# Optimization experiments

Measured on AMD Instinct MI355X. Metric: run time of the kernel, lower is better.

Reference implementation:

```python
import jax, jax.numpy as jnp
import numpy as np

N_NODES = 50000
N_EDGES = 640000
IN_F, HID, OUT = 128, 128, 64
EPS = 1e-5


def _glorot(key, shape):
    fan_in, fan_out = shape
    lim = jnp.sqrt(6.0 / (fan_in + fan_out))
    return jax.random.uniform(key, shape, jnp.float32, -lim, lim)


def setup_inputs() -> dict:
    key = jax.random.key(0)
    ks = jax.random.split(key, 16)
    inp = {
        "x": jax.random.normal(ks[0], (N_NODES, IN_F), jnp.float32),
        "src": jax.random.randint(ks[1], (N_EDGES,), 0, N_NODES, jnp.int32),
        "dst": jax.random.randint(ks[2], (N_EDGES,), 0, N_NODES, jnp.int32),
        # layer 0: in -> hid
        "Ws0": _glorot(ks[3], (IN_F, HID)),
        "Wn0": _glorot(ks[4], (IN_F, HID)),
        "b0": jnp.zeros((HID,), jnp.float32),
        # layer 1: hid -> hid
        "Ws1": _glorot(ks[5], (HID, HID)),
        "Wn1": _glorot(ks[6], (HID, HID)),
        "b1": jnp.zeros((HID,), jnp.float32),
        # layer 2: hid -> out
        "Ws2": _glorot(ks[7], (HID, OUT)),
        "Wn2": _glorot(ks[8], (HID, OUT)),
        "b2": jnp.zeros((OUT,), jnp.float32),
        # batchnorm params for the two hidden layers
        "g0": jnp.ones((HID,), jnp.float32),
        "beta0": jnp.zeros((HID,), jnp.float32),
        "g1": jnp.ones((HID,), jnp.float32),
        "beta1": jnp.zeros((HID,), jnp.float32),
    }
    return inp


def _sage_conv(h, src, dst, Ws, Wn, b):
    # mean aggregation over in-neighbors (DGL SAGEConv 'mean')
    ones = jnp.ones_like(dst, dtype=h.dtype)
    deg = jax.ops.segment_sum(ones, dst, num_segments=N_NODES)
    agg = jax.ops.segment_sum(h[src], dst, num_segments=N_NODES)
    agg = agg / jnp.maximum(deg, 1.0)[:, None]
    return h @ Ws + agg @ Wn + b


def _batchnorm(h, gamma, beta):
    mu = jnp.mean(h, axis=0)
    var = jnp.mean(jnp.square(h - mu), axis=0)  # biased, like torch BN
    return (h - mu) * jax.lax.rsqrt(var + EPS) * gamma + beta


def reference(x, src, dst, Ws0, Wn0, b0, Ws1, Wn1, b1, Ws2, Wn2, b2,
              g0, beta0, g1, beta1):
    h = _sage_conv(x, src, dst, Ws0, Wn0, b0)
    h = jax.nn.relu(_batchnorm(h, g0, beta0))  # dropout = identity (eval)
    h = _sage_conv(h, src, dst, Ws1, Wn1, b1)
    h = jax.nn.relu(_batchnorm(h, g1, beta1))
    h = _sage_conv(h, src, dst, Ws2, Wn2, b2)
    return h
```

## Files before the change

### kernel.cpp

```cpp
#include <hip/hip_runtime.h>

#define N_NODES 50000
#define N_EDGES 640000
#define EPS 1e-5f
#define NBLK_SCAN 196
#define CGRID 3125

typedef __attribute__((ext_vector_type(8))) short short8;
typedef __attribute__((ext_vector_type(4))) float f32x4;

__device__ inline unsigned short f2bf(float f) {
    unsigned u = __float_as_uint(f);
    u += 0x7fffu + ((u >> 16) & 1u);
    return (unsigned short)(u >> 16);
}
__device__ inline float bf2f(unsigned short b) {
    return __uint_as_float(((unsigned)b) << 16);
}
__device__ inline void storev(short* p, float v) { *(unsigned short*)p = f2bf(v); }
__device__ inline void storev(float* p, float v) { *p = v; }

__global__ void hist_kernel(const int* __restrict__ dst, int* __restrict__ counts,
                            int* __restrict__ erank) {
    int i = blockIdx.x * 256 + threadIdx.x;
    if (i >= N_EDGES / 8) return;
    int4 a = ((const int4*)dst)[2 * i];
    int4 b = ((const int4*)dst)[2 * i + 1];
    int4 ra, rb;
    ra.x = atomicAdd(&counts[a.x], 1);
    ra.y = atomicAdd(&counts[a.y], 1);
    ra.z = atomicAdd(&counts[a.z], 1);
    ra.w = atomicAdd(&counts[a.w], 1);
    rb.x = atomicAdd(&counts[b.x], 1);
    rb.y = atomicAdd(&counts[b.y], 1);
    rb.z = atomicAdd(&counts[b.z], 1);
    rb.w = atomicAdd(&counts[b.w], 1);
    ((int4*)erank)[2 * i]     = ra;
    ((int4*)erank)[2 * i + 1] = rb;
}

__global__ void scan1_kernel(const int* __restrict__ counts, int* __restrict__ incl,
                             int* __restrict__ bsums) {
    __shared__ int tmp[256];
    int t = threadIdx.x;
    int i = blockIdx.x * 256 + t;
    tmp[t] = (i < N_NODES) ? counts[i] : 0;
    __syncthreads();
    for (int off = 1; off < 256; off <<= 1) {
        int add = (t >= off) ? tmp[t - off] : 0;
        __syncthreads();
        tmp[t] += add;
        __syncthreads();
    }
    if (i < N_NODES) incl[i] = tmp[t];
    if (t == 255) bsums[blockIdx.x] = tmp[255];
}

__global__ void scan2_kernel(const int* __restrict__ bsums, int* __restrict__ boff) {
    __shared__ int tmp[256];
    int t = threadIdx.x;
    tmp[t] = (t < NBLK_SCAN) ? bsums[t] : 0;
    __syncthreads();
    for (int off = 1; off < 256; off <<= 1) {
        int add = (t >= off) ? tmp[t - off] : 0;
        __syncthreads();
        tmp[t] += add;
        __syncthreads();
    }
    if (t < NBLK_SCAN) boff[t] = (t == 0) ? 0 : tmp[t - 1];
}

__global__ void scan3_kernel(const int* __restrict__ counts, const int* __restrict__ incl,
                             const int* __restrict__ boff, int* __restrict__ rowptr,
                             float* __restrict__ rdeg) {
    int i = blockIdx.x * 256 + threadIdx.x;
    if (i >= N_NODES) return;
    int c = counts[i];
    int inc = incl[i] + boff[blockIdx.x];
    rowptr[i] = inc - c;
    rdeg[i] = 1.0f / fmaxf((float)c, 1.0f);
    if (i == N_NODES - 1) rowptr[N_NODES] = inc;
}

__global__ void fill_kernel(const int* __restrict__ src, const int* __restrict__ dst,
                            const int* __restrict__ erank, const int* __restrict__ rowptr,
                            int* __restrict__ esrc) {
    int i = blockIdx.x * 256 + threadIdx.x;
    if (i >= N_EDGES / 8) return;
    int4 da = ((const int4*)dst)[2 * i];
    int4 db = ((const int4*)dst)[2 * i + 1];
    int4 sa = ((const int4*)src)[2 * i];
    int4 sb = ((const int4*)src)[2 * i + 1];
    int4 ra = ((const int4*)erank)[2 * i];
    int4 rb = ((const int4*)erank)[2 * i + 1];
    esrc[rowptr[da.x] + ra.x] = sa.x;
    esrc[rowptr[da.y] + ra.y] = sa.y;
    esrc[rowptr[da.z] + ra.z] = sa.z;
    esrc[rowptr[da.w] + ra.w] = sa.w;
    esrc[rowptr[db.x] + rb.x] = sb.x;
    esrc[rowptr[db.y] + rb.y] = sb.y;
    esrc[rowptr[db.z] + rb.z] = sb.z;
    esrc[rowptr[db.w] + rb.w] = sb.w;
}

__global__ void prep_kernel(const float* __restrict__ in, short* __restrict__ outp,
                            int* __restrict__ counts, float* __restrict__ stats,
                            const float* __restrict__ W0, const float* __restrict__ W1,
                            const float* __restrict__ W2, const float* __restrict__ W3,
                            const float* __restrict__ W4, const float* __restrict__ W5,
                            short* __restrict__ P0, short* __restrict__ P1,
                            short* __restrict__ P2, short* __restrict__ P3,
                            short* __restrict__ P4, short* __restrict__ P5) {
    int bi = blockIdx.x, t = threadIdx.x;
    if (bi < CGRID) {
        if (bi == 0 && t < 128) {
            float4 z = make_float4(0.f, 0.f, 0.f, 0.f);
            ((float4*)stats)[t] = z;
        }
        if (bi >= 1 && bi <= NBLK_SCAN) {
            int idx = (bi - 1) * 256 + t;
            if (idx < N_NODES) counts[idx] = 0;
        }
        int i = bi * 256 + t;
        if (i >= N_NODES * 16) return;
        const float4* p = (const float4*)in + 2 * (size_t)i;
        float4 a = p[0], b = p[1];
        short8 v;
        v[0] = (short)f2bf(a.x); v[1] = (short)f2bf(a.y);
        v[2] = (short)f2bf(a.z); v[3] = (short)f2bf(a.w);
        v[4] = (short)f2bf(b.x); v[5] = (short)f2bf(b.y);
        v[6] = (short)f2bf(b.z); v[7] = (short)f2bf(b.w);
        *((short8*)outp + i) = v;
        return;
    }
    int b = bi - CGRID;
    const float* W; short* P; int NC; int base;
    if      (b < 8)  { W = W0; P = P0; NC = 128; base = 0;  }
    else if (b < 16) { W = W1; P = P1; NC = 128; base = 8;  }
    else if (b < 24) { W = W2; P = P2; NC = 128; base = 16; }
    else if (b < 32) { W = W3; P = P3; NC = 128; base = 24; }
    else if (b < 36) { W = W4; P = P4; NC = 64;  base = 32; }
    else             { W = W5; P = P5; NC = 64;  base = 36; }
    int idx = (b - base) * 256 + t;
    int total = 4 * (NC / 16) * 64;
    if (idx >= total) return;
    int lane = idx & 63;
    int cbks = idx >> 6;
    int cb = cbks % (NC / 16);
    int ks = cbks / (NC / 16);
    int col = cb * 16 + (lane & 15);
    int k0 = ks * 32 + ((lane >> 4) << 3);
    short8 v;
    #pragma unroll
    for (int j = 0; j < 8; ++j) v[j] = (short)f2bf(W[(size_t)(k0 + j) * NC + col]);
    *((short8*)P + idx) = v;
}

template<bool BN>
__global__ void gather_k(const short* __restrict__ h, const int* __restrict__ rowptr,
                         const int* __restrict__ esrc, const float* __restrict__ rdeg,
                         const float* __restrict__ sums, const float* __restrict__ sqs,
                         const float* __restrict__ g, const float* __restrict__ beta,
                         short* __restrict__ agg) {
    int node = blockIdx.x * 4 + (threadIdx.x >> 6);
    int lane = threadIdx.x & 63;
    if (node >= N_NODES) return;
    int beg = rowptr[node], end = rowptr[node + 1];
    float s0 = 0.f, s1 = 0.f, b0 = 0.f, b1 = 0.f;
    if (BN) {
        const float invN = 1.0f / N_NODES;
        float2 sm = *(const float2*)(sums + lane * 2);
        float2 sq = *(const float2*)(sqs + lane * 2);
        float2 gg = *(const float2*)(g + lane * 2);
        float2 bb = *(const float2*)(beta + lane * 2);
        float m0 = sm.x * invN, m1 = sm.y * invN;
        float v0 = sq.x * invN - m0 * m0, v1 = sq.y * invN - m1 * m1;
        s0 = rsqrtf(v0 + EPS) * gg.x;
        s1 = rsqrtf(v1 + EPS) * gg.y;
        b0 = bb.x - m0 * s0;
        b1 = bb.y - m1 * s1;
    }
    float ax = 0.f, ay = 0.f;
    while (beg < end) {
        int cnt = min(end - beg, 64);
        int mi = esrc[beg + min(lane, cnt - 1)];
        for (int j = 0; j < cnt; j += 16) {
            int lim = cnt - j; if (lim > 16) lim = 16;
            unsigned v[16];
            #pragma unroll
            for (int u = 0; u < 16; ++u) {
                int s = __shfl(mi, j + (u < lim ? u : lim - 1));
                v[u] = *(const unsigned*)(h + (size_t)s * 128 + lane * 2);
            }
            #pragma unroll
            for (int u = 0; u < 16; ++u) {
                if (u < lim) {
                    float lo = __uint_as_float(v[u] << 16);
                    float hi = __uint_as_float(v[u] & 0xffff0000u);
                    if (BN) {
                        lo = fmaxf(fmaf(lo, s0, b0), 0.f);
                        hi = fmaxf(fmaf(hi, s1, b1), 0.f);
                    }
                    ax += lo; ay += hi;
                }
            }
        }
        beg += cnt;
    }
    float r = rdeg[node];
    unsigned o = ((unsigned)f2bf(ay * r) << 16) | (unsigned)f2bf(ax * r);
    *(unsigned*)(agg + (size_t)node * 128 + lane * 2) = o;
}

template<int NC, bool BNIN, bool STATS, typename OUT>
__global__ __launch_bounds__(512, 4)
void sage_mfma(const short* __restrict__ h, const short* __restrict__ agg,
               const short* __restrict__ Wpk,
               const float* __restrict__ bias,
               const float* __restrict__ sums_in, const float* __restrict__ sqs_in,
               const float* __restrict__ g_in, const float* __restrict__ beta_in,
               float* __restrict__ sums, float* __restrict__ sqs,
               OUT* __restrict__ out) {
    constexpr int CBF = NC / 16;
    constexpr int WSH8 = CBF * 256;
    __shared__ short8 wlds[2 * WSH8];
    __shared__ float ls[128], lq[128];
    const int t = threadIdx.x;
    const int lane = t & 63;
    const int w = t >> 6;
    const int wrow = blockIdx.x * 128 + w * 16;
    const int arow = wrow + (lane & 15);
    const int koff = (lane >> 4) << 3;

    {
        const short8* gw = (const short8*)Wpk;
        #pragma unroll
        for (int i = 0; i < (2 * WSH8) / 512; ++i)
            wlds[t + i * 512] = gw[t + i * 512];
    }
    if (BNIN) {
        if (t < 128) {
            const float invN = 1.0f / N_NODES;
            float m = sums_in[t] * invN;
            float v = sqs_in[t] * invN - m * m;
            float sc = rsqrtf(v + EPS) * g_in[t];
            ls[t] = sc;
            lq[t] = beta_in[t] - m * sc;
        }
    }
    __syncthreads();

    short8 zero8 = {0, 0, 0, 0, 0, 0, 0, 0};
    short8 A[8];
    if (arow < N_NODES) {
        const short8* hb = (const short8*)(h + (size_t)arow * 128 + koff);
        const short8* ab = (const short8*)(agg + (size_t)arow * 128 + koff);
        #pragma unroll
        for (int ks = 0; ks < 4; ++ks) {
            A[ks] = hb[ks * 4];
            A[4 + ks] = ab[ks * 4];
        }
        if (BNIN) {
            #pragma unroll
            for (int ks = 0; ks < 4; ++ks) {
                int base = ks * 32 + koff;
                float4 sc0 = *(const float4*)&ls[base];
                float4 sc1 = *(const float4*)&ls[base + 4];
                float4 sh0 = *(const float4*)&lq[base];
                float4 sh1 = *(const float4*)&lq[base + 4];
                float scv[8] = {sc0.x, sc0.y, sc0.z, sc0.w, sc1.x, sc1.y, sc1.z, sc1.w};
                float shv[8] = {sh0.x, sh0.y, sh0.z, sh0.w, sh1.x, sh1.y, sh1.z, sh1.w};
                short8 v = A[ks];
                #pragma unroll
                for (int j = 0; j < 8; ++j) {
                    float f = bf2f((unsigned short)v[j]);
                    f = fmaxf(fmaf(f, scv[j], shv[j]), 0.f);
                    v[j] = (short)f2bf(f);
                }
                A[ks] = v;
            }
        }
    } else {
        #pragma unroll
        for (int s = 0; s < 8; ++s) A[s] = zero8;
    }

    if (STATS) {
        if (BNIN) __syncthreads();
        if (t < NC) { ls[t] = 0.f; lq[t] = 0.f; }
        __syncthreads();
    }

    f32x4 zacc = {0.f, 0.f, 0.f, 0.f};
    f32x4 acc[CBF];
    #pragma unroll
    for (int c = 0; c < CBF; ++c) acc[c] = zacc;

    #pragma unroll
    for (int s = 0; s < 8; ++s) {
        const int base = (s < 4) ? s * CBF * 64 : WSH8 + (s - 4) * CBF * 64;
        short8 af = A[s];
        #pragma unroll
        for (int c = 0; c < CBF; ++c) {
            short8 b = wlds[base + c * 64 + lane];
            acc[c] = __builtin_amdgcn_mfma_f32_16x16x32_bf16(af, b, acc[c], 0, 0, 0);
        }
    }

    const int col16 = lane & 15;
    const int rbase = wrow + ((lane >> 4) << 2);
    #pragma unroll
    for (int c = 0; c < CBF; ++c) {
        int gcol = c * 16 + col16;
        float bb = bias[gcol];
        float ps = 0.f, pq = 0.f;
        #pragma unroll
        for (int r = 0; r < 4; ++r) {
            int row = rbase + r;
            if (row < N_NODES) {
                float val = acc[c][r] + bb;
                storev(out + (size_t)row * NC + gcol, val);
                if (STATS) { ps += val; pq += val * val; }
            }
        }
        if (STATS) {
            ps += __shfl_xor(ps, 16); ps += __shfl_xor(ps, 32);
            pq += __shfl_xor(pq, 16); pq += __shfl_xor(pq, 32);
            if (lane < 16) {
                atomicAdd(&ls[gcol], ps);
                atomicAdd(&lq[gcol], pq);
            }
        }
    }
    if (STATS) {
        __syncthreads();
        if (t < NC) {
            atomicAdd(&sums[t], ls[t]);
            atomicAdd(&sqs[t], lq[t]);
        }
    }
}

__global__ __launch_bounds__(512, 4)
void sage_mfma2(const short* __restrict__ h, const short* __restrict__ Wpk,
                const float* __restrict__ bias,
                const float* __restrict__ sums_in, const float* __restrict__ sqs_in,
                const float* __restrict__ g_in, const float* __restrict__ beta_in,
                float* __restrict__ out, short* __restrict__ z2) {
    constexpr int CBF = 4;
    constexpr int WSH8 = 1024;
    __shared__ short8 wlds[2 * WSH8];
    __shared__ float ls[128], lq[128];
    const int t = threadIdx.x;
    const int lane = t & 63;
    const int w = t >> 6;
    const int wrow = blockIdx.x * 128 + w * 16;
    const int arow = wrow + (lane & 15);
    const int koff = (lane >> 4) << 3;

    {
        const short8* gw = (const short8*)Wpk;
        #pragma unroll
        for (int i = 0; i < (2 * WSH8) / 512; ++i)
            wlds[t + i * 512] = gw[t + i * 512];
    }
    if (t < 128) {
        const float invN = 1.0f / N_NODES;
        float m = sums_in[t] * invN;
        float v = sqs_in[t] * invN - m * m;
        float sc = rsqrtf(v + EPS) * g_in[t];
        ls[t] = sc;
        lq[t] = beta_in[t] - m * sc;
    }
    __syncthreads();

    short8 zero8 = {0, 0, 0, 0, 0, 0, 0, 0};
    short8 A[4];
    if (arow < N_NODES) {
        const short8* hb = (const short8*)(h + (size_t)arow * 128 + koff);
        #pragma unroll
        for (int ks = 0; ks < 4; ++ks) {
            int base = ks * 32 + koff;
            float4 sc0 = *(const float4*)&ls[base];
            float4 sc1 = *(const float4*)&ls[base + 4];
            float4 sh0 = *(const float4*)&lq[base];
            float4 sh1 = *(const float4*)&lq[base + 4];
            float scv[8] = {sc0.x, sc0.y, sc0.z, sc0.w, sc1.x, sc1.y, sc1.z, sc1.w};
            float shv[8] = {sh0.x, sh0.y, sh0.z, sh0.w, sh1.x, sh1.y, sh1.z, sh1.w};
            short8 v = hb[ks * 4];
            #pragma unroll
            for (int j = 0; j < 8; ++j) {
                float f = bf2f((unsigned short)v[j]);
                f = fmaxf(fmaf(f, scv[j], shv[j]), 0.f);
                v[j] = (short)f2bf(f);
            }
            A[ks] = v;
        }
    } else {
        #pragma unroll
        for (int s = 0; s < 4; ++s) A[s] = zero8;
    }

    f32x4 zacc = {0.f, 0.f, 0.f, 0.f};
    f32x4 accy[CBF], accz[CBF];
    #pragma unroll
    for (int c = 0; c < CBF; ++c) { accy[c] = zacc; accz[c] = zacc; }

    #pragma unroll
    for (int s = 0; s < 4; ++s) {
        short8 af = A[s];
        #pragma unroll
        for (int c = 0; c < CBF; ++c) {
            short8 by = wlds[s * 256 + c * 64 + lane];
            accy[c] = __builtin_amdgcn_mfma_f32_16x16x32_bf16(af, by, accy[c], 0, 0, 0);
        }
        #pragma unroll
        for (int c = 0; c < CBF; ++c) {
            short8 bz = wlds[WSH8 + s * 256 + c * 64 + lane];
            accz[c] = __builtin_amdgcn_mfma_f32_16x16x32_bf16(af, bz, accz[c], 0, 0, 0);
        }
    }

    const int col16 = lane & 15;
    const int rbase = wrow + ((lane >> 4) << 2);
    #pragma unroll
    for (int c = 0; c < CBF; ++c) {
        int gcol = c * 16 + col16;
        float bb = bias[gcol];
        #pragma unroll
        for (int r = 0; r < 4; ++r) {
            int row = rbase + r;
            if (row < N_NODES) {
                out[(size_t)row * 64 + gcol] = accy[c][r] + bb;
                storev(z2 + (size_t)row * 64 + gcol, accz[c][r]);
            }
        }
    }
}

__global__ void gather64_add(const short* __restrict__ z2, const int* __restrict__ rowptr,
                             const int* __restrict__ esrc, const float* __restrict__ rdeg,
                             float* __restrict__ out) {
    int node = blockIdx.x * 4 + (threadIdx.x >> 6);
    int lane = threadIdx.x & 63;
    if (node >= N_NODES) return;
    const int e = lane >> 5;
    const int p = lane & 31;
    int beg = rowptr[node], end = rowptr[node + 1];
    float a0 = 0.f, a1 = 0.f;
    while (beg < end) {
        int cnt = min(end - beg, 64);
        int mi = esrc[beg + min(lane, cnt - 1)];
        for (int j = 0; j < cnt; j += 16) {
            unsigned v[8];
            #pragma unroll
            for (int u = 0; u < 8; ++u) {
                int idx = j + 2 * u + e;
                int s = __shfl(mi, min(idx, cnt - 1));
                v[u] = *(const unsigned*)(z2 + (size_t)s * 64 + p * 2);
            }
            #pragma unroll
            for (int u = 0; u < 8; ++u) {
                int idx = j + 2 * u + e;
                if (idx < cnt) {
                    a0 += __uint_as_float(v[u] << 16);
                    a1 += __uint_as_float(v[u] & 0xffff0000u);
                }
            }
        }
        beg += cnt;
    }
    a0 += __shfl_xor(a0, 32);
    a1 += __shfl_xor(a1, 32);
    if (e == 0) {
        float r = rdeg[node];
        float2* po = (float2*)(out + (size_t)node * 64 + p * 2);
        float2 y = *po;
        y.x += a0 * r;
        y.y += a1 * r;
        *po = y;
    }
}

extern "C" void kernel_launch(void* const* d_in, const int* in_sizes, int n_in,
                              void* d_out, int out_size, void* d_ws, size_t ws_size,
                              hipStream_t stream) {
    const float* x   = (const float*)d_in[0];
    const int*   src = (const int*)d_in[1];
    const int*   dst = (const int*)d_in[2];
    const float* Ws0 = (const float*)d_in[3];
    const float* Wn0 = (const float*)d_in[4];
    const float* b0  = (const float*)d_in[5];
    const float* Ws1 = (const float*)d_in[6];
    const float* Wn1 = (const float*)d_in[7];
    const float* b1  = (const float*)d_in[8];
    const float* Ws2 = (const float*)d_in[9];
    const float* Wn2 = (const float*)d_in[10];
    const float* b2  = (const float*)d_in[11];
    const float* g0  = (const float*)d_in[12];
    const float* bt0 = (const float*)d_in[13];
    const float* g1  = (const float*)d_in[14];
    const float* bt1 = (const float*)d_in[15];

    char* ws = (char*)d_ws;
    const size_t HB2 = (size_t)N_NODES * 128 * 2;
    size_t off = 0;
    short* xb     = (short*)(ws + off); off += HB2;
    short* aggb   = (short*)(ws + off); off += HB2;
    short* h1b    = (short*)(ws + off); off += HB2;
    short* h2b    = (short*)(ws + off); off += HB2;
    short* z2b    = (short*)(ws + off); off += (size_t)N_NODES * 64 * 2;
    int*   esrc   = (int*)(ws + off);   off += (size_t)N_EDGES * 4;
    int*   erank  = (int*)(ws + off);   off += (size_t)N_EDGES * 4;
    int*   counts = (int*)(ws + off);   off += 200192;
    int*   incl   = (int*)(ws + off);   off += 200192;
    int*   rowptr = (int*)(ws + off);   off += 200704;
    float* rdeg   = (float*)(ws + off); off += 200192;
    int*   bsums  = (int*)(ws + off);   off += 1024;
    int*   boff   = (int*)(ws + off);   off += 1024;
    float* stats  = (float*)(ws + off); off += 2048;
    float* sums0  = stats;
    float* sqs0   = stats + 128;
    float* sums1  = stats + 256;
    float* sqs1   = stats + 384;
    short* pW0    = (short*)(ws + off); off += 65536;
    short* pW1    = (short*)(ws + off); off += 65536;
    short* pW2    = (short*)(ws + off); off += 32768;

    float* out = (float*)d_out;

    const int e8grid = (N_EDGES / 8 + 255) / 256;
    const int ggrid  = (N_NODES + 3) / 4;
    const int mgrid  = (N_NODES + 127) / 128;

    prep_kernel<<<CGRID + 40, 256, 0, stream>>>(
        x, xb, counts, stats, Ws0, Wn0, Ws1, Wn1, Ws2, Wn2,
        pW0, pW0 + 16384, pW1, pW1 + 16384, pW2, pW2 + 8192);
    hist_kernel<<<e8grid, 256, 0, stream>>>(dst, counts, erank);
    scan1_kernel<<<NBLK_SCAN, 256, 0, stream>>>(counts, incl, bsums);
    scan2_kernel<<<1, 256, 0, stream>>>(bsums, boff);
    scan3_kernel<<<NBLK_SCAN, 256, 0, stream>>>(counts, incl, boff, rowptr, rdeg);
    fill_kernel<<<e8grid, 256, 0, stream>>>(src, dst, erank, rowptr, esrc);

    gather_k<false><<<ggrid, 256, 0, stream>>>(xb, rowptr, esrc, rdeg,
                                               nullptr, nullptr, nullptr, nullptr, aggb);
    sage_mfma<128, false, true, short><<<mgrid, 512, 0, stream>>>(
        xb, aggb, pW0, b0, nullptr, nullptr, nullptr, nullptr, sums0, sqs0, h1b);

    gather_k<true><<<ggrid, 256, 0, stream>>>(h1b, rowptr, esrc, rdeg,
                                              sums0, sqs0, g0, bt0, aggb);
    sage_mfma<128, true, true, short><<<mgrid, 512, 0, stream>>>(
        h1b, aggb, pW1, b1, sums0, sqs0, g0, bt0, sums1, sqs1, h2b);

    sage_mfma2<<<mgrid, 512, 0, stream>>>(
        h2b, pW2, b2, sums1, sqs1, g1, bt1, out, z2b);
    gather64_add<<<ggrid, 256, 0, stream>>>(z2b, rowptr, esrc, rdeg, out);
}
```

Before: 193.5 us.

## Split node features into 32-column quarter planes for cache-local gathers

Feature matrices (bf16 x, h1, h2, agg, z2) are stored as separate 32-column planes, each covering all nodes, instead of row-major 128-wide rows. The gather kernels now launch one grid slice per plane, so each pass touches a 3.2 MB working set that fits in cache better. Each wave handles four edges at once with 16 lanes per row, then reduces with shuffles. The MFMA kernels read and write with the new plane strides. The cost is more blocks and re-reading the edge index and rowptr arrays once per plane.

After: 309.2 us. 1.6x slower.

```diff
diff --git a/kernel.cpp b/kernel.cpp
--- a/kernel.cpp
+++ b/kernel.cpp
@@ -5,6 +5,7 @@
 #define EPS 1e-5f
 #define NBLK_SCAN 196
 #define CGRID 3125
+#define GQB 12500
 
 typedef __attribute__((ext_vector_type(8))) short short8;
 typedef __attribute__((ext_vector_type(4))) float f32x4;
@@ -111,6 +112,7 @@
                             short* __restrict__ P0, short* __restrict__ P1,
                             short* __restrict__ P2, short* __restrict__ P3,
                             short* __restrict__ P4, short* __restrict__ P5) {
+    const size_t QS = (size_t)N_NODES * 32;
     int bi = blockIdx.x, t = threadIdx.x;
     if (bi < CGRID) {
         if (bi == 0 && t < 128) {
@@ -130,7 +132,8 @@
         v[2] = (short)f2bf(a.z); v[3] = (short)f2bf(a.w);
         v[4] = (short)f2bf(b.x); v[5] = (short)f2bf(b.y);
         v[6] = (short)f2bf(b.z); v[7] = (short)f2bf(b.w);
-        *((short8*)outp + i) = v;
+        int row = i >> 4, c8 = i & 15;
+        *(short8*)(outp + QS * (c8 >> 2) + (size_t)row * 32 + (c8 & 3) * 8) = v;
         return;
     }
     int b = bi - CGRID;
@@ -157,22 +160,29 @@
 }
 
 template<bool BN>
-__global__ void gather_k(const short* __restrict__ h, const int* __restrict__ rowptr,
+__global__ void gather_q(const short* __restrict__ hq_base, const int* __restrict__ rowptr,
                          const int* __restrict__ esrc, const float* __restrict__ rdeg,
                          const float* __restrict__ sums, const float* __restrict__ sqs,
                          const float* __restrict__ g, const float* __restrict__ beta,
-                         short* __restrict__ agg) {
-    int node = blockIdx.x * 4 + (threadIdx.x >> 6);
+                         short* __restrict__ agg_base) {
+    const size_t QS = (size_t)N_NODES * 32;
+    int bq = blockIdx.x / GQB;
+    int nb = blockIdx.x % GQB;
+    int node = nb * 4 + (threadIdx.x >> 6);
     int lane = threadIdx.x & 63;
-    if (node >= N_NODES) return;
-    int beg = rowptr[node], end = rowptr[node + 1];
+    const int e = lane >> 4;
+    const int p = lane & 15;
+    const short* hq = hq_base + QS * bq;
+    short* aggq = agg_base + QS * bq;
+
     float s0 = 0.f, s1 = 0.f, b0 = 0.f, b1 = 0.f;
     if (BN) {
         const float invN = 1.0f / N_NODES;
-        float2 sm = *(const float2*)(sums + lane * 2);
-        float2 sq = *(const float2*)(sqs + lane * 2);
-        float2 gg = *(const float2*)(g + lane * 2);
-        float2 bb = *(const float2*)(beta + lane * 2);
+        int c = bq * 32 + p * 2;
+        float2 sm = *(const float2*)(sums + c);
+        float2 sq = *(const float2*)(sqs + c);
+        float2 gg = *(const float2*)(g + c);
+        float2 bb = *(const float2*)(beta + c);
         float m0 = sm.x * invN, m1 = sm.y * invN;
         float v0 = sq.x * invN - m0 * m0, v1 = sq.y * invN - m1 * m1;
         s0 = rsqrtf(v0 + EPS) * gg.x;
@@ -180,39 +190,39 @@
         b0 = bb.x - m0 * s0;
         b1 = bb.y - m1 * s1;
     }
-    float ax = 0.f, ay = 0.f;
+
+    int beg = rowptr[node], end = rowptr[node + 1];
+    float a0 = 0.f, a1 = 0.f;
     while (beg < end) {
         int cnt = min(end - beg, 64);
         int mi = esrc[beg + min(lane, cnt - 1)];
-        for (int j = 0; j < cnt; j += 16) {
-            int lim = cnt - j; if (lim > 16) lim = 16;
-            unsigned v[16];
-            #pragma unroll
-            for (int u = 0; u < 16; ++u) {
-                int s = __shfl(mi, j + (u < lim ? u : lim - 1));
-                v[u] = *(const unsigned*)(h + (size_t)s * 128 + lane * 2);
-            }
-            #pragma unroll
-            for (int u = 0; u < 16; ++u) {
-                if (u < lim) {
-                    float lo = __uint_as_float(v[u] << 16);
-                    float hi = __uint_as_float(v[u] & 0xffff0000u);
-                    if (BN) {
-                        lo = fmaxf(fmaf(lo, s0, b0), 0.f);
-                        hi = fmaxf(fmaf(hi, s1, b1), 0.f);
-                    }
-                    ax += lo; ay += hi;
+        #pragma unroll 4
+        for (int j = 0; j < cnt; j += 4) {
+            int idx = j + e;
+            int s = __shfl(mi, min(idx, cnt - 1));
+            unsigned v = *(const unsigned*)(hq + (size_t)s * 32 + p * 2);
+            if (idx < cnt) {
+                float lo = __uint_as_float(v << 16);
+                float hi = __uint_as_float(v & 0xffff0000u);
+                if (BN) {
+                    lo = fmaxf(fmaf(lo, s0, b0), 0.f);
+                    hi = fmaxf(fmaf(hi, s1, b1), 0.f);
                 }
+                a0 += lo; a1 += hi;
             }
         }
         beg += cnt;
     }
-    float r = rdeg[node];
-    unsigned o = ((unsigned)f2bf(ay * r) << 16) | (unsigned)f2bf(ax * r);
-    *(unsigned*)(agg + (size_t)node * 128 + lane * 2) = o;
-}
-
-template<int NC, bool BNIN, bool STATS, typename OUT>
+    a0 += __shfl_xor(a0, 16); a0 += __shfl_xor(a0, 32);
+    a1 += __shfl_xor(a1, 16); a1 += __shfl_xor(a1, 32);
+    if (e == 0) {
+        float r = rdeg[node];
+        unsigned o = ((unsigned)f2bf(a1 * r) << 16) | (unsigned)f2bf(a0 * r);
+        __builtin_nontemporal_store(o, (unsigned*)(aggq + (size_t)node * 32 + p * 2));
+    }
+}
+
+template<int NC, bool BNIN, bool STATS>
 __global__ __launch_bounds__(512, 4)
 void sage_mfma(const short* __restrict__ h, const short* __restrict__ agg,
                const short* __restrict__ Wpk,
@@ -220,7 +230,8 @@
                const float* __restrict__ sums_in, const float* __restrict__ sqs_in,
                const float* __restrict__ g_in, const float* __restrict__ beta_in,
                float* __restrict__ sums, float* __restrict__ sqs,
-               OUT* __restrict__ out) {
+               short* __restrict__ out) {
+    const size_t QS = (size_t)N_NODES * 32;
     constexpr int CBF = NC / 16;
     constexpr int WSH8 = CBF * 256;
     __shared__ short8 wlds[2 * WSH8];
@@ -253,12 +264,10 @@
     short8 zero8 = {0, 0, 0, 0, 0, 0, 0, 0};
     short8 A[8];
     if (arow < N_NODES) {
-        const short8* hb = (const short8*)(h + (size_t)arow * 128 + koff);
-        const short8* ab = (const short8*)(agg + (size_t)arow * 128 + koff);
         #pragma unroll
         for (int ks = 0; ks < 4; ++ks) {
-            A[ks] = hb[ks * 4];
-            A[4 + ks] = ab[ks * 4];
+            A[ks]     = *(const short8*)(h   + QS * ks + (size_t)arow * 32 + koff);
+            A[4 + ks] = *(const short8*)(agg + QS * ks + (size_t)arow * 32 + koff);
         }
         if (BNIN) {
             #pragma unroll
@@ -314,12 +323,14 @@
         int gcol = c * 16 + col16;
         float bb = bias[gcol];
         float ps = 0.f, pq = 0.f;
+        short* obase = out + QS * (c >> 1);
+        int ocol = (c & 1) * 16 + col16;
         #pragma unroll
         for (int r = 0; r < 4; ++r) {
             int row = rbase + r;
             if (row < N_NODES) {
                 float val = acc[c][r] + bb;
-                storev(out + (size_t)row * NC + gcol, val);
+                storev(obase + (size_t)row * 32 + ocol, val);
                 if (STATS) { ps += val; pq += val * val; }
             }
         }
@@ -347,6 +358,7 @@
                 const float* __restrict__ sums_in, const float* __restrict__ sqs_in,
                 const float* __restrict__ g_in, const float* __restrict__ beta_in,
                 float* __restrict__ out, short* __restrict__ z2) {
+    const size_t QS = (size_t)N_NODES * 32;
     constexpr int CBF = 4;
     constexpr int WSH8 = 1024;
     __shared__ short8 wlds[2 * WSH8];
@@ -377,7 +389,6 @@
     short8 zero8 = {0, 0, 0, 0, 0, 0, 0, 0};
     short8 A[4];
     if (arow < N_NODES) {
-        const short8* hb = (const short8*)(h + (size_t)arow * 128 + koff);
         #pragma unroll
         for (int ks = 0; ks < 4; ++ks) {
             int base = ks * 32 + koff;
@@ -387,7 +398,7 @@
             float4 sh1 = *(const float4*)&lq[base + 4];
             float scv[8] = {sc0.x, sc0.y, sc0.z, sc0.w, sc1.x, sc1.y, sc1.z, sc1.w};
             float shv[8] = {sh0.x, sh0.y, sh0.z, sh0.w, sh1.x, sh1.y, sh1.z, sh1.w};
-            short8 v = hb[ks * 4];
+            short8 v = *(const short8*)(h + QS * ks + (size_t)arow * 32 + koff);
             #pragma unroll
             for (int j = 0; j < 8; ++j) {
                 float f = bf2f((unsigned short)v[j]);
@@ -427,54 +438,53 @@
     for (int c = 0; c < CBF; ++c) {
         int gcol = c * 16 + col16;
         float bb = bias[gcol];
+        short* zbase = z2 + QS * (c >> 1);
+        int ocol = (c & 1) * 16 + col16;
         #pragma unroll
         for (int r = 0; r < 4; ++r) {
             int row = rbase + r;
             if (row < N_NODES) {
                 out[(size_t)row * 64 + gcol] = accy[c][r] + bb;
-                storev(z2 + (size_t)row * 64 + gcol, accz[c][r]);
-            }
-        }
-    }
-}
-
-__global__ void gather64_add(const short* __restrict__ z2, const int* __restrict__ rowptr,
+                storev(zbase + (size_t)row * 32 + ocol, accz[c][r]);
+            }
+        }
+    }
+}
+
+__global__ void gather32_add(const short* __restrict__ z2, const int* __restrict__ rowptr,
                              const int* __restrict__ esrc, const float* __restrict__ rdeg,
                              float* __restrict__ out) {
-    int node = blockIdx.x * 4 + (threadIdx.x >> 6);
+    const size_t QS = (size_t)N_NODES * 32;
+    int bq = blockIdx.x / GQB;
+    int nb = blockIdx.x % GQB;
+    int node = nb * 4 + (threadIdx.x >> 6);
     int lane = threadIdx.x & 63;
-    if (node >= N_NODES) return;
-    const int e = lane >> 5;
-    const int p = lane & 31;
+    const int e = lane >> 4;
+    const int p = lane & 15;
+    const short* zq = z2 + QS * bq;
+
     int beg = rowptr[node], end = rowptr[node + 1];
     float a0 = 0.f, a1 = 0.f;
     while (beg < end) {
         int cnt = min(end - beg, 64);
         int mi = esrc[beg + min(lane, cnt - 1)];
-        for (int j = 0; j < cnt; j += 16) {
-            unsigned v[8];
-            #pragma unroll
-            for (int u = 0; u < 8; ++u) {
-                int idx = j + 2 * u + e;
-                int s = __shfl(mi, min(idx, cnt - 1));
-                v[u] = *(const unsigned*)(z2 + (size_t)s * 64 + p * 2);
-            }
-            #pragma unroll
-            for (int u = 0; u < 8; ++u) {
-                int idx = j + 2 * u + e;
-                if (idx < cnt) {
-                    a0 += __uint_as_float(v[u] << 16);
-                    a1 += __uint_as_float(v[u] & 0xffff0000u);
-                }
+        #pragma unroll 4
+        for (int j = 0; j < cnt; j += 4) {
+            int idx = j + e;
+            int s = __shfl(mi, min(idx, cnt - 1));
+            unsigned v = *(const unsigned*)(zq + (size_t)s * 32 + p * 2);
+            if (idx < cnt) {
+                a0 += __uint_as_float(v << 16);
+                a1 += __uint_as_float(v & 0xffff0000u);
             }
         }
         beg += cnt;
     }
-    a0 += __shfl_xor(a0, 32);
-    a1 += __shfl_xor(a1, 32);
+    a0 += __shfl_xor(a0, 16); a0 += __shfl_xor(a0, 32);
+    a1 += __shfl_xor(a1, 16); a1 += __shfl_xor(a1, 32);
     if (e == 0) {
         float r = rdeg[node];
-        float2* po = (float2*)(out + (size_t)node * 64 + p * 2);
+        float2* po = (float2*)(out + (size_t)node * 64 + bq * 32 + p * 2);
         float2 y = *po;
         y.x += a0 * r;
         y.y += a1 * r;
@@ -530,7 +540,6 @@
     float* out = (float*)d_out;
 
     const int e8grid = (N_EDGES / 8 + 255) / 256;
-    const int ggrid  = (N_NODES + 3) / 4;
     const int mgrid  = (N_NODES + 127) / 128;
 
     prep_kernel<<<CGRID + 40, 256, 0, stream>>>(
@@ -542,17 +551,17 @@
     scan3_kernel<<<NBLK_SCAN, 256, 0, stream>>>(counts, incl, boff, rowptr, rdeg);
     fill_kernel<<<e8grid, 256, 0, stream>>>(src, dst, erank, rowptr, esrc);
 
-    gather_k<false><<<ggrid, 256, 0, stream>>>(xb, rowptr, esrc, rdeg,
-                                               nullptr, nullptr, nullptr, nullptr, aggb);
-    sage_mfma<128, false, true, short><<<mgrid, 512, 0, stream>>>(
+    gather_q<false><<<4 * GQB, 256, 0, stream>>>(xb, rowptr, esrc, rdeg,
+                                                 nullptr, nullptr, nullptr, nullptr, aggb);
+    sage_mfma<128, false, true><<<mgrid, 512, 0, stream>>>(
         xb, aggb, pW0, b0, nullptr, nullptr, nullptr, nullptr, sums0, sqs0, h1b);
 
-    gather_k<true><<<ggrid, 256, 0, stream>>>(h1b, rowptr, esrc, rdeg,
-                                              sums0, sqs0, g0, bt0, aggb);
-    sage_mfma<128, true, true, short><<<mgrid, 512, 0, stream>>>(
+    gather_q<true><<<4 * GQB, 256, 0, stream>>>(h1b, rowptr, esrc, rdeg,
+                                                sums0, sqs0, g0, bt0, aggb);
+    sage_mfma<128, true, true><<<mgrid, 512, 0, stream>>>(
         h1b, aggb, pW1, b1, sums0, sqs0, g0, bt0, sums1, sqs1, h2b);
 
     sage_mfma2<<<mgrid, 512, 0, stream>>>(
         h2b, pW2, b2, sums1, sqs1, g1, bt1, out, z2b);
-    gather64_add<<<ggrid, 256, 0, stream>>>(z2b, rowptr, esrc, rdeg, out);
-}
+    gather32_add<<<2 * GQB, 256, 0, stream>>>(z2b, rowptr, esrc, rdeg, out);
+}
```
